# Kernel optimization log

Hardware: AMD Instinct MI355X
Metric: run time of the kernel (lower is better)

The kernel has to match this reference:

```python
import jax, jax.numpy as jnp
import numpy as np

M, L, D, V = 4096, 15, 1024, 32  # moves, word_max, in_sz, vocab_sz


def setup_inputs() -> dict:
    key = jax.random.key(0)
    ks = jax.random.split(key, 9)
    s = 0.02
    return {
        "tokens": jax.random.randint(ks[0], (M, L), 0, V),
        "letter_emb": jax.random.normal(ks[1], (V, D), jnp.float32) * s,
        "pos_emb": jax.random.normal(ks[2], (L, D), jnp.float32) * s,
        "Wq": jax.random.normal(ks[3], (D, D), jnp.float32) * s,
        "bq": jax.random.normal(ks[4], (D,), jnp.float32) * s,
        "Wk": jax.random.normal(ks[5], (D, D), jnp.float32) * s,
        "bk": jax.random.normal(ks[6], (D,), jnp.float32) * s,
        "Wv": jax.random.normal(ks[7], (D, D), jnp.float32) * s,
        "bv": jax.random.normal(ks[8], (D,), jnp.float32) * s,
    }


def reference(tokens, letter_emb, pos_emb, Wq, bq, Wk, bk, Wv, bv):
    # WordEncoder, batched across all M moves.
    x = letter_emb[tokens] + pos_emb[None, :, :]          # [M, L, D]
    q = jnp.einsum("mld,ed->mle", x, Wq) + bq             # Linear: x @ W.T + b
    k = jnp.einsum("mld,ed->mle", x, Wk) + bk
    v = jnp.einsum("mld,ed->mle", x, Wv) + bv
    scores = jax.nn.softmax(jnp.einsum("mle,mke->mlk", q, k), axis=-1)  # [M, L, L]
    attn = jnp.einsum("mlk,mke->mle", scores, v)          # [M, L, D]
    word = attn.sum(axis=1)                               # [M, D]
    # enc = word + ordered, where ordered is an identical second evaluation
    # of word_enc on the same word -> enc = 2 * word.
    return 2.0 * word
```

## Files before the change

kernel.cpp:

```cpp
#include <hip/hip_runtime.h>
#include <hip/hip_bf16.h>

#define NMOVES 4096
#define LW     15
#define DIM    1024
#define VOC    32
#define XROW   48
#define KSPL   4
#define GSPL   8
#define PLSZ   (48 * DIM)

typedef __attribute__((ext_vector_type(8))) short  short8;
typedef __attribute__((ext_vector_type(4))) float  floatx4;

__device__ __forceinline__ unsigned short f2b(float f) {
  unsigned int x;
  __builtin_memcpy(&x, &f, 4);
  x = x + 0x7FFFu + ((x >> 16) & 1u);
  return (unsigned short)(x >> 16);
}
__device__ __forceinline__ float b2f(unsigned short u) {
  unsigned int x = ((unsigned int)u) << 16;
  float f;
  __builtin_memcpy(&f, &x, 4);
  return f;
}
__device__ __forceinline__ short8 pk8(float4 a, float4 b) {
  short8 r;
  r[0] = (short)f2b(a.x); r[1] = (short)f2b(a.y);
  r[2] = (short)f2b(a.z); r[3] = (short)f2b(a.w);
  r[4] = (short)f2b(b.x); r[5] = (short)f2b(b.y);
  r[6] = (short)f2b(b.z); r[7] = (short)f2b(b.w);
  return r;
}
__device__ __forceinline__ float4 ld4(const float* p) {
  return *reinterpret_cast<const float4*>(p);
}

__global__ __launch_bounds__(256) void proj_ksplit(
    const float* __restrict__ letter, const float* __restrict__ pos,
    const float* __restrict__ Wq, const float* __restrict__ Wk,
    const float* __restrict__ Wv, float* __restrict__ Xp,
    float* __restrict__ G48) {
  const int tid = threadIdx.x;
  if (blockIdx.x == 0 && blockIdx.y == 0 && blockIdx.z == 0) {
#pragma unroll
    for (int i = 0; i < (XROW * 64) / 256; ++i) G48[i * 256 + tid] = 0.f;
  }

  const int p     = blockIdx.x;
  const int bn0   = blockIdx.y * 64;
  const int z     = blockIdx.z;
  const int kbase = p * 256;
  const float* W = (z == 0) ? Wq : (z == 1) ? Wk : Wv;
  float*       O = Xp + (size_t)(z * KSPL + p) * PLSZ;

  const int lane = tid & 63;
  const int wave = tid >> 6;
  const int wr   = wave >> 1;
  const int wc   = wave & 1;
  const int quad = lane >> 4;
  const int l16  = lane & 15;

  const int rA0 = wr * 32 + l16;
  const int rA1 = rA0 + 16;
  const float* a0p = (rA0 < 32) ? letter + (size_t)rA0 * DIM
                   : (rA0 < 47) ? pos + (size_t)(rA0 - 32) * DIM : nullptr;
  const float* a1p = (rA1 < 32) ? letter + (size_t)rA1 * DIM
                   : (rA1 < 47) ? pos + (size_t)(rA1 - 32) * DIM : nullptr;
  const float* b0p = W + (size_t)(bn0 + wc * 32 + l16) * DIM;
  const float* b1p = b0p + (size_t)16 * DIM;

  floatx4 acc[2][2];
#pragma unroll
  for (int i = 0; i < 2; ++i)
#pragma unroll
    for (int j = 0; j < 2; ++j) acc[i][j] = (floatx4){0.f, 0.f, 0.f, 0.f};

  const short8 z8 = (short8){0,0,0,0,0,0,0,0};
#pragma unroll
  for (int kk = 0; kk < 256; kk += 32) {
    const int kc = kbase + kk + quad * 8;
    short8 a0 = a0p ? pk8(ld4(a0p + kc), ld4(a0p + kc + 4)) : z8;
    short8 a1 = a1p ? pk8(ld4(a1p + kc), ld4(a1p + kc + 4)) : z8;
    short8 b0 = pk8(ld4(b0p + kc), ld4(b0p + kc + 4));
    short8 b1 = pk8(ld4(b1p + kc), ld4(b1p + kc + 4));
    acc[0][0] = __builtin_amdgcn_mfma_f32_16x16x32_bf16(a0, b0, acc[0][0], 0, 0, 0);
    acc[0][1] = __builtin_amdgcn_mfma_f32_16x16x32_bf16(a0, b1, acc[0][1], 0, 0, 0);
    acc[1][0] = __builtin_amdgcn_mfma_f32_16x16x32_bf16(a1, b0, acc[1][0], 0, 0, 0);
    acc[1][1] = __builtin_amdgcn_mfma_f32_16x16x32_bf16(a1, b1, acc[1][1], 0, 0, 0);
  }

#pragma unroll
  for (int mi = 0; mi < 2; ++mi) {
#pragma unroll
    for (int ni = 0; ni < 2; ++ni) {
      const int gcol = bn0 + wc * 32 + ni * 16 + l16;
#pragma unroll
      for (int i = 0; i < 4; ++i) {
        const int grow = wr * 32 + mi * 16 + quad * 4 + i;
        if (grow < 47)
          O[(size_t)grow * DIM + gcol] = acc[mi][ni][i];
      }
    }
  }
}

__device__ __forceinline__ short8 gfrag(const float* __restrict__ X4,
                                        const float* __restrict__ bias,
                                        int row, int kc) {
  if (row < 47) {
    const float* r0 = X4 + (size_t)row * DIM + kc;
    float4 s0 = ld4(r0),            s1 = ld4(r0 + 4);
    float4 t0 = ld4(r0 + PLSZ),     t1 = ld4(r0 + PLSZ + 4);
    float4 u0 = ld4(r0 + 2 * PLSZ), u1 = ld4(r0 + 2 * PLSZ + 4);
    float4 v0 = ld4(r0 + 3 * PLSZ), v1 = ld4(r0 + 3 * PLSZ + 4);
    s0.x += t0.x + u0.x + v0.x; s0.y += t0.y + u0.y + v0.y;
    s0.z += t0.z + u0.z + v0.z; s0.w += t0.w + u0.w + v0.w;
    s1.x += t1.x + u1.x + v1.x; s1.y += t1.y + u1.y + v1.y;
    s1.z += t1.z + u1.z + v1.z; s1.w += t1.w + u1.w + v1.w;
    return pk8(s0, s1);
  } else if (row == 47) {
    return pk8(ld4(bias + kc), ld4(bias + kc + 4));
  }
  return (short8){0,0,0,0,0,0,0,0};
}

__global__ __launch_bounds__(256) void gram_vexp(
    const float* __restrict__ Xp,
    const float* __restrict__ bq, const float* __restrict__ bk,
    float* __restrict__ G48, unsigned short* __restrict__ XvT) {
  const int bid = blockIdx.x;
  const int tid = threadIdx.x;

  if (bid < GSPL) {
    const int kbase = bid * 128;
    const int lane = tid & 63;
    const int wave = tid >> 6;
    const int wr   = wave >> 1;
    const int wc   = wave & 1;
    const int quad = lane >> 4;
    const int l16  = lane & 15;

    const float* Xq4 = Xp;
    const float* Xk4 = Xp + (size_t)4 * PLSZ;
    const int rA0 = wr * 32 + l16, rA1 = rA0 + 16;
    const int rB0 = wc * 32 + l16, rB1 = rB0 + 16;

    floatx4 acc[2][2];
#pragma unroll
    for (int i = 0; i < 2; ++i)
#pragma unroll
      for (int j = 0; j < 2; ++j) acc[i][j] = (floatx4){0.f, 0.f, 0.f, 0.f};

#pragma unroll
    for (int kk = 0; kk < 128; kk += 32) {
      const int kc = kbase + kk + quad * 8;
      short8 a0 = gfrag(Xq4, bq, rA0, kc);
      short8 a1 = gfrag(Xq4, bq, rA1, kc);
      short8 b0 = gfrag(Xk4, bk, rB0, kc);
      short8 b1 = gfrag(Xk4, bk, rB1, kc);
      acc[0][0] = __builtin_amdgcn_mfma_f32_16x16x32_bf16(a0, b0, acc[0][0], 0, 0, 0);
      acc[0][1] = __builtin_amdgcn_mfma_f32_16x16x32_bf16(a0, b1, acc[0][1], 0, 0, 0);
      acc[1][0] = __builtin_amdgcn_mfma_f32_16x16x32_bf16(a1, b0, acc[1][0], 0, 0, 0);
      acc[1][1] = __builtin_amdgcn_mfma_f32_16x16x32_bf16(a1, b1, acc[1][1], 0, 0, 0);
    }

#pragma unroll
    for (int mi = 0; mi < 2; ++mi) {
#pragma unroll
      for (int ni = 0; ni < 2; ++ni) {
        const int gcol = wc * 32 + ni * 16 + l16;
#pragma unroll
        for (int i = 0; i < 4; ++i) {
          const int grow = wr * 32 + mi * 16 + quad * 4 + i;
          if (grow < XROW)
            atomicAdd(&G48[(size_t)grow * 64 + gcol], acc[mi][ni][i]);
        }
      }
    }
  } else {
    const int n  = (bid - GSPL) * 64 + (tid & 63);
    const int kg = tid >> 6;
    const float* Xv4 = Xp + (size_t)8 * PLSZ;
#pragma unroll
    for (int s = 0; s < 4; ++s) {
      const int k0 = kg * 4 + s * 16;
      ushort4 o;
      unsigned short* oc = &o.x;
#pragma unroll
      for (int i = 0; i < 4; ++i) {
        const int k = k0 + i;
        float v = 0.f;
        if (k < 47) {
          const size_t off = (size_t)k * DIM + n;
          v = Xv4[off] + Xv4[off + PLSZ] + Xv4[off + 2 * PLSZ] +
              Xv4[off + 3 * PLSZ];
        }
        oc[i] = f2b(v);
      }
      *reinterpret_cast<ushort4*>(XvT + (size_t)n * 64 + k0) = o;
    }
  }
}

__global__ __launch_bounds__(256) void attn_gemm(
    const void* __restrict__ tokens_raw, const float* __restrict__ G48,
    const unsigned short* __restrict__ XvT, const float* __restrict__ bv,
    float* __restrict__ out) {
  __shared__ float Gs[XROW * 65];
  __shared__ float Sm[16][LW][17];
  __shared__ float CL[16][64];
  __shared__ __attribute__((aligned(16))) unsigned short CLh[16 * 72];
  __shared__ __attribute__((aligned(16))) unsigned short CLl[16 * 72];
  __shared__ int   tokL[16][16];
  __shared__ int   is64_s;
  const int m0  = blockIdx.x * 16;
  const int cb0 = blockIdx.y * 256;
  const int tid = threadIdx.x;

  const unsigned int* u32 = (const unsigned int*)tokens_raw;
  if (tid < 64) {
    unsigned int v = u32[2 * tid + 1];
    unsigned long long nz = __ballot(v != 0);
    if (tid == 0) is64_s = (nz == 0ULL) ? 1 : 0;
  }
#pragma unroll
  for (int i = 0; i < 12; ++i) {
    const int idx = i * 256 + tid;
    Gs[(idx >> 6) * 65 + (idx & 63)] = G48[idx];
  }
  {
    const int g = tid >> 4, L = tid & 15;
#pragma unroll
    for (int i = 0; i < 4; ++i) CL[g][L * 4 + i] = 0.f;
  }
  __syncthreads();

  if (tid < 16 * LW) {
    const int mv = tid / LW, j = tid - mv * LW;
    int t;
    if (is64_s) t = (int)((const long long*)tokens_raw)[(size_t)(m0 + mv) * LW + j];
    else        t = ((const int*)tokens_raw)[(size_t)(m0 + mv) * LW + j];
    tokL[mv][j] = t;
  }
  __syncthreads();

  const int g = tid >> 4;
  const int L = tid & 15;
  if (L < LW) {
    const int rb0 = tokL[g][L] * 65;
    const int rb1 = (32 + L) * 65;
    const int rb2 = (XROW - 1) * 65;
    float S[LW];
#pragma unroll
    for (int j = 0; j < LW; ++j) {
      const int c0 = tokL[g][j];
      const int c1 = 32 + j;
      S[j] = Gs[rb0 + c0] + Gs[rb1 + c0] + Gs[rb2 + c0]
           + Gs[rb0 + c1] + Gs[rb1 + c1] + Gs[rb2 + c1];
    }
    float mx = S[0];
#pragma unroll
    for (int j = 1; j < LW; ++j) mx = fmaxf(mx, S[j]);
    float sum = 0.f;
#pragma unroll
    for (int j = 0; j < LW; ++j) { S[j] = __expf(S[j] - mx); sum += S[j]; }
    const float inv = 1.0f / sum;
#pragma unroll
    for (int j = 0; j < LW; ++j) Sm[g][L][j] = S[j] * inv;
  }
  __syncthreads();

  if (L < LW) {
    float s = 0.f;
#pragma unroll
    for (int l = 0; l < LW; ++l) s += Sm[g][l][L];
    const float wj = 2.0f * s;
    atomicAdd(&CL[g][tokL[g][L]], wj);
    CL[g][32 + L] = wj;
  }
  __syncthreads();

  {
    float4 cv = *reinterpret_cast<const float4*>(&CL[g][L * 4]);
    ushort4 hi, lo;
    hi.x = f2b(cv.x); hi.y = f2b(cv.y); hi.z = f2b(cv.z); hi.w = f2b(cv.w);
    lo.x = f2b(cv.x - b2f(hi.x)); lo.y = f2b(cv.y - b2f(hi.y));
    lo.z = f2b(cv.z - b2f(hi.z)); lo.w = f2b(cv.w - b2f(hi.w));
    *reinterpret_cast<ushort4*>(CLh + g * 72 + L * 4) = hi;
    *reinterpret_cast<ushort4*>(CLl + g * 72 + L * 4) = lo;
  }
  __syncthreads();

  const int lane = tid & 63;
  const int wave = tid >> 6;
  const int quad = lane >> 4;
  const int l16  = lane & 15;
  const int colb = cb0 + wave * 64;

  floatx4 acc[4];
#pragma unroll
  for (int i = 0; i < 4; ++i) acc[i] = (floatx4){0.f, 0.f, 0.f, 0.f};

#pragma unroll
  for (int ks = 0; ks < 64; ks += 32) {
    short8 ah = *reinterpret_cast<const short8*>(CLh + l16 * 72 + ks + quad * 8);
    short8 al = *reinterpret_cast<const short8*>(CLl + l16 * 72 + ks + quad * 8);
#pragma unroll
    for (int ni = 0; ni < 4; ++ni) {
      const unsigned short* B = XvT + (size_t)(colb + ni * 16 + l16) * 64;
      short8 b = *reinterpret_cast<const short8*>(B + ks + quad * 8);
      acc[ni] = __builtin_amdgcn_mfma_f32_16x16x32_bf16(ah, b, acc[ni], 0, 0, 0);
      acc[ni] = __builtin_amdgcn_mfma_f32_16x16x32_bf16(al, b, acc[ni], 0, 0, 0);
    }
  }

#pragma unroll
  for (int ni = 0; ni < 4; ++ni) {
    const int gcol = colb + ni * 16 + l16;
    const float bias30 = 30.0f * bv[gcol];
#pragma unroll
    for (int i = 0; i < 4; ++i) {
      out[(size_t)(m0 + quad * 4 + i) * DIM + gcol] = acc[ni][i] + bias30;
    }
  }
}

extern "C" void kernel_launch(void* const* d_in, const int* in_sizes, int n_in,
                              void* d_out, int out_size, void* d_ws, size_t ws_size,
                              hipStream_t stream) {
  const void*  tokens = d_in[0];
  const float* letter = (const float*)d_in[1];
  const float* pos    = (const float*)d_in[2];
  const float* Wq     = (const float*)d_in[3];
  const float* bq     = (const float*)d_in[4];
  const float* Wk     = (const float*)d_in[5];
  const float* bk     = (const float*)d_in[6];
  const float* Wv     = (const float*)d_in[7];
  const float* bv     = (const float*)d_in[8];
  float*       outp   = (float*)d_out;

  char* ws = (char*)d_ws;
  const size_t XP_SZ  = (size_t)12 * PLSZ * 4;
  const size_t G_SZ   = (size_t)XROW * 64 * 4;
  float*          Xp  = (float*)(ws);
  float*          Gp  = (float*)(ws + XP_SZ);
  unsigned short* XvT = (unsigned short*)(ws + XP_SZ + G_SZ);

  proj_ksplit<<<dim3(KSPL, 16, 3), 256, 0, stream>>>(letter, pos, Wq, Wk, Wv,
                                                     Xp, Gp);
  gram_vexp<<<GSPL + 16, 256, 0, stream>>>(Xp, bq, bk, Gp, XvT);
  attn_gemm<<<dim3(NMOVES / 16, 4), 256, 0, stream>>>(tokens, Gp, XvT, bv, outp);
}
```

Before: 113.9 us.

## Fuse projection and gram kernels with a grid-wide atomic barrier

Merges the k-split projection kernel and the gram/V-transpose kernel into one launch. Producer blocks increment a global counter after writing partial projections, and consumer blocks spin until all 192 producers are done. This removes one kernel launch and the inter-kernel gap. The cost is spin-wait overhead, and it relies on all blocks being co-resident. The counter reset combined with persistent magic words may race across repeated calls.

Measured after the change: 121.5 us. 1.07x slower.

```diff
diff --git a/kernel.cpp b/kernel.cpp
--- a/kernel.cpp
+++ b/kernel.cpp
@@ -9,6 +9,7 @@
 #define KSPL   4
 #define GSPL   8
 #define PLSZ   (48 * DIM)
+#define ARM_MAGIC 0xA17C0DE1u
 
 typedef __attribute__((ext_vector_type(8))) short  short8;
 typedef __attribute__((ext_vector_type(4))) float  floatx4;
@@ -35,75 +36,6 @@
 }
 __device__ __forceinline__ float4 ld4(const float* p) {
   return *reinterpret_cast<const float4*>(p);
-}
-
-__global__ __launch_bounds__(256) void proj_ksplit(
-    const float* __restrict__ letter, const float* __restrict__ pos,
-    const float* __restrict__ Wq, const float* __restrict__ Wk,
-    const float* __restrict__ Wv, float* __restrict__ Xp,
-    float* __restrict__ G48) {
-  const int tid = threadIdx.x;
-  if (blockIdx.x == 0 && blockIdx.y == 0 && blockIdx.z == 0) {
-#pragma unroll
-    for (int i = 0; i < (XROW * 64) / 256; ++i) G48[i * 256 + tid] = 0.f;
-  }
-
-  const int p     = blockIdx.x;
-  const int bn0   = blockIdx.y * 64;
-  const int z     = blockIdx.z;
-  const int kbase = p * 256;
-  const float* W = (z == 0) ? Wq : (z == 1) ? Wk : Wv;
-  float*       O = Xp + (size_t)(z * KSPL + p) * PLSZ;
-
-  const int lane = tid & 63;
-  const int wave = tid >> 6;
-  const int wr   = wave >> 1;
-  const int wc   = wave & 1;
-  const int quad = lane >> 4;
-  const int l16  = lane & 15;
-
-  const int rA0 = wr * 32 + l16;
-  const int rA1 = rA0 + 16;
-  const float* a0p = (rA0 < 32) ? letter + (size_t)rA0 * DIM
-                   : (rA0 < 47) ? pos + (size_t)(rA0 - 32) * DIM : nullptr;
-  const float* a1p = (rA1 < 32) ? letter + (size_t)rA1 * DIM
-                   : (rA1 < 47) ? pos + (size_t)(rA1 - 32) * DIM : nullptr;
-  const float* b0p = W + (size_t)(bn0 + wc * 32 + l16) * DIM;
-  const float* b1p = b0p + (size_t)16 * DIM;
-
-  floatx4 acc[2][2];
-#pragma unroll
-  for (int i = 0; i < 2; ++i)
-#pragma unroll
-    for (int j = 0; j < 2; ++j) acc[i][j] = (floatx4){0.f, 0.f, 0.f, 0.f};
-
-  const short8 z8 = (short8){0,0,0,0,0,0,0,0};
-#pragma unroll
-  for (int kk = 0; kk < 256; kk += 32) {
-    const int kc = kbase + kk + quad * 8;
-    short8 a0 = a0p ? pk8(ld4(a0p + kc), ld4(a0p + kc + 4)) : z8;
-    short8 a1 = a1p ? pk8(ld4(a1p + kc), ld4(a1p + kc + 4)) : z8;
-    short8 b0 = pk8(ld4(b0p + kc), ld4(b0p + kc + 4));
-    short8 b1 = pk8(ld4(b1p + kc), ld4(b1p + kc + 4));
-    acc[0][0] = __builtin_amdgcn_mfma_f32_16x16x32_bf16(a0, b0, acc[0][0], 0, 0, 0);
-    acc[0][1] = __builtin_amdgcn_mfma_f32_16x16x32_bf16(a0, b1, acc[0][1], 0, 0, 0);
-    acc[1][0] = __builtin_amdgcn_mfma_f32_16x16x32_bf16(a1, b0, acc[1][0], 0, 0, 0);
-    acc[1][1] = __builtin_amdgcn_mfma_f32_16x16x32_bf16(a1, b1, acc[1][1], 0, 0, 0);
-  }
-
-#pragma unroll
-  for (int mi = 0; mi < 2; ++mi) {
-#pragma unroll
-    for (int ni = 0; ni < 2; ++ni) {
-      const int gcol = bn0 + wc * 32 + ni * 16 + l16;
-#pragma unroll
-      for (int i = 0; i < 4; ++i) {
-        const int grow = wr * 32 + mi * 16 + quad * 4 + i;
-        if (grow < 47)
-          O[(size_t)grow * DIM + gcol] = acc[mi][ni][i];
-      }
-    }
-  }
 }
 
 __device__ __forceinline__ short8 gfrag(const float* __restrict__ X4,
@@ -126,15 +58,37 @@
   return (short8){0,0,0,0,0,0,0,0};
 }
 
-__global__ __launch_bounds__(256) void gram_vexp(
-    const float* __restrict__ Xp,
+__global__ __launch_bounds__(256) void proj_gram(
+    const float* __restrict__ letter, const float* __restrict__ pos,
+    const float* __restrict__ Wq, const float* __restrict__ Wk,
+    const float* __restrict__ Wv,
     const float* __restrict__ bq, const float* __restrict__ bk,
-    float* __restrict__ G48, unsigned short* __restrict__ XvT) {
+    float* __restrict__ Xp, float* __restrict__ G48,
+    unsigned short* __restrict__ XvT, unsigned int* __restrict__ syncw) {
   const int bid = blockIdx.x;
   const int tid = threadIdx.x;
 
-  if (bid < GSPL) {
-    const int kbase = bid * 128;
+  if (bid < 192) {
+    if (bid == 0) {
+#pragma unroll
+      for (int i = 0; i < (XROW * 64) / 256; ++i) G48[i * 256 + tid] = 0.f;
+      __syncthreads();
+      if (tid == 0) {
+        atomicExch(&syncw[0], 0u);
+        __threadfence();
+        atomicExch(&syncw[2], ARM_MAGIC);
+        atomicExch(&syncw[3], ~ARM_MAGIC);
+      }
+    }
+
+    const int p  = bid & 3;
+    const int ny = (bid >> 2) & 15;
+    const int z  = bid >> 6;
+    const int kbase = p * 256;
+    const int bn0   = ny * 64;
+    const float* W = (z == 0) ? Wq : (z == 1) ? Wk : Wv;
+    float*       O = Xp + (size_t)(z * KSPL + p) * PLSZ;
+
     const int lane = tid & 63;
     const int wave = tid >> 6;
     const int wr   = wave >> 1;
@@ -142,10 +96,14 @@
     const int quad = lane >> 4;
     const int l16  = lane & 15;
 
-    const float* Xq4 = Xp;
-    const float* Xk4 = Xp + (size_t)4 * PLSZ;
-    const int rA0 = wr * 32 + l16, rA1 = rA0 + 16;
-    const int rB0 = wc * 32 + l16, rB1 = rB0 + 16;
+    const int rA0 = wr * 32 + l16;
+    const int rA1 = rA0 + 16;
+    const float* a0p = (rA0 < 32) ? letter + (size_t)rA0 * DIM
+                     : (rA0 < 47) ? pos + (size_t)(rA0 - 32) * DIM : nullptr;
+    const float* a1p = (rA1 < 32) ? letter + (size_t)rA1 * DIM
+                     : (rA1 < 47) ? pos + (size_t)(rA1 - 32) * DIM : nullptr;
+    const float* b0p = W + (size_t)(bn0 + wc * 32 + l16) * DIM;
+    const float* b1p = b0p + (size_t)16 * DIM;
 
     floatx4 acc[2][2];
 #pragma unroll
@@ -153,13 +111,14 @@
 #pragma unroll
       for (int j = 0; j < 2; ++j) acc[i][j] = (floatx4){0.f, 0.f, 0.f, 0.f};
 
-#pragma unroll
-    for (int kk = 0; kk < 128; kk += 32) {
+    const short8 z8 = (short8){0,0,0,0,0,0,0,0};
+#pragma unroll
+    for (int kk = 0; kk < 256; kk += 32) {
       const int kc = kbase + kk + quad * 8;
-      short8 a0 = gfrag(Xq4, bq, rA0, kc);
-      short8 a1 = gfrag(Xq4, bq, rA1, kc);
-      short8 b0 = gfrag(Xk4, bk, rB0, kc);
-      short8 b1 = gfrag(Xk4, bk, rB1, kc);
+      short8 a0 = a0p ? pk8(ld4(a0p + kc), ld4(a0p + kc + 4)) : z8;
+      short8 a1 = a1p ? pk8(ld4(a1p + kc), ld4(a1p + kc + 4)) : z8;
+      short8 b0 = pk8(ld4(b0p + kc), ld4(b0p + kc + 4));
+      short8 b1 = pk8(ld4(b1p + kc), ld4(b1p + kc + 4));
       acc[0][0] = __builtin_amdgcn_mfma_f32_16x16x32_bf16(a0, b0, acc[0][0], 0, 0, 0);
       acc[0][1] = __builtin_amdgcn_mfma_f32_16x16x32_bf16(a0, b1, acc[0][1], 0, 0, 0);
       acc[1][0] = __builtin_amdgcn_mfma_f32_16x16x32_bf16(a1, b0, acc[1][0], 0, 0, 0);
@@ -170,36 +129,101 @@
     for (int mi = 0; mi < 2; ++mi) {
 #pragma unroll
       for (int ni = 0; ni < 2; ++ni) {
-        const int gcol = wc * 32 + ni * 16 + l16;
+        const int gcol = bn0 + wc * 32 + ni * 16 + l16;
 #pragma unroll
         for (int i = 0; i < 4; ++i) {
           const int grow = wr * 32 + mi * 16 + quad * 4 + i;
-          if (grow < XROW)
-            atomicAdd(&G48[(size_t)grow * 64 + gcol], acc[mi][ni][i]);
+          if (grow < 47)
+            O[(size_t)grow * DIM + gcol] = acc[mi][ni][i];
         }
       }
     }
+
+    __syncthreads();
+    if (tid == 0) {
+      while (atomicAdd(&syncw[2], 0u) != ARM_MAGIC ||
+             atomicAdd(&syncw[3], 0u) != ~ARM_MAGIC) { }
+      __threadfence();
+      atomicAdd(&syncw[0], 1u);
+    }
   } else {
-    const int n  = (bid - GSPL) * 64 + (tid & 63);
-    const int kg = tid >> 6;
-    const float* Xv4 = Xp + (size_t)8 * PLSZ;
-#pragma unroll
-    for (int s = 0; s < 4; ++s) {
-      const int k0 = kg * 4 + s * 16;
-      ushort4 o;
-      unsigned short* oc = &o.x;
-#pragma unroll
-      for (int i = 0; i < 4; ++i) {
-        const int k = k0 + i;
-        float v = 0.f;
-        if (k < 47) {
-          const size_t off = (size_t)k * DIM + n;
-          v = Xv4[off] + Xv4[off + PLSZ] + Xv4[off + 2 * PLSZ] +
-              Xv4[off + 3 * PLSZ];
+    if (tid == 0) {
+      while (atomicAdd(&syncw[2], 0u) != ARM_MAGIC ||
+             atomicAdd(&syncw[3], 0u) != ~ARM_MAGIC) { }
+      while (atomicAdd(&syncw[0], 0u) < 192u) { }
+      __threadfence();
+    }
+    __syncthreads();
+
+    const int cb = bid - 192;
+    if (cb < GSPL) {
+      const int kbase = cb * 128;
+      const int lane = tid & 63;
+      const int wave = tid >> 6;
+      const int wr   = wave >> 1;
+      const int wc   = wave & 1;
+      const int quad = lane >> 4;
+      const int l16  = lane & 15;
+
+      const float* Xq4 = Xp;
+      const float* Xk4 = Xp + (size_t)4 * PLSZ;
+      const int rA0 = wr * 32 + l16, rA1 = rA0 + 16;
+      const int rB0 = wc * 32 + l16, rB1 = rB0 + 16;
+
+      floatx4 acc[2][2];
+#pragma unroll
+      for (int i = 0; i < 2; ++i)
+#pragma unroll
+        for (int j = 0; j < 2; ++j) acc[i][j] = (floatx4){0.f, 0.f, 0.f, 0.f};
+
+#pragma unroll
+      for (int kk = 0; kk < 128; kk += 32) {
+        const int kc = kbase + kk + quad * 8;
+        short8 a0 = gfrag(Xq4, bq, rA0, kc);
+        short8 a1 = gfrag(Xq4, bq, rA1, kc);
+        short8 b0 = gfrag(Xk4, bk, rB0, kc);
+        short8 b1 = gfrag(Xk4, bk, rB1, kc);
+        acc[0][0] = __builtin_amdgcn_mfma_f32_16x16x32_bf16(a0, b0, acc[0][0], 0, 0, 0);
+        acc[0][1] = __builtin_amdgcn_mfma_f32_16x16x32_bf16(a0, b1, acc[0][1], 0, 0, 0);
+        acc[1][0] = __builtin_amdgcn_mfma_f32_16x16x32_bf16(a1, b0, acc[1][0], 0, 0, 0);
+        acc[1][1] = __builtin_amdgcn_mfma_f32_16x16x32_bf16(a1, b1, acc[1][1], 0, 0, 0);
+      }
+
+#pragma unroll
+      for (int mi = 0; mi < 2; ++mi) {
+#pragma unroll
+        for (int ni = 0; ni < 2; ++ni) {
+          const int gcol = wc * 32 + ni * 16 + l16;
+#pragma unroll
+          for (int i = 0; i < 4; ++i) {
+            const int grow = wr * 32 + mi * 16 + quad * 4 + i;
+            if (grow < XROW)
+              atomicAdd(&G48[(size_t)grow * 64 + gcol], acc[mi][ni][i]);
+          }
         }
-        oc[i] = f2b(v);
-      }
-      *reinterpret_cast<ushort4*>(XvT + (size_t)n * 64 + k0) = o;
+      }
+    } else {
+      const int n  = (cb - GSPL) * 64 + (tid & 63);
+      const int kg = tid >> 6;
+      const float* Xv4 = Xp + (size_t)8 * PLSZ;
+#pragma unroll
+      for (int s = 0; s < 4; ++s) {
+        const int k0 = kg * 4 + s * 16;
+        ushort4 o;
+        unsigned short* oc = &o.x;
+#pragma unroll
+        for (int i = 0; i < 4; ++i) {
+          const int k = k0 + i;
+          float v = 0.f;
+          if (k < 47) {
+            const size_t off = (size_t)k * DIM + n;
+            v = Xv4[off] + Xv4[off + PLSZ] + Xv4[off + 2 * PLSZ] +
+                Xv4[off + 3 * PLSZ];
+          }
+          oc[i] = f2b(v);
+        }
+        *reinterpret_cast<ushort4*>(XvT + (size_t)n * 64 + k0) = o;
+      }
     }
   }
 }
@@ -344,12 +368,13 @@
   char* ws = (char*)d_ws;
   const size_t XP_SZ  = (size_t)12 * PLSZ * 4;
   const size_t G_SZ   = (size_t)XROW * 64 * 4;
-  float*          Xp  = (float*)(ws);
-  float*          Gp  = (float*)(ws + XP_SZ);
-  unsigned short* XvT = (unsigned short*)(ws + XP_SZ + G_SZ);
-
-  proj_ksplit<<<dim3(KSPL, 16, 3), 256, 0, stream>>>(letter, pos, Wq, Wk, Wv,
-                                                     Xp, Gp);
-  gram_vexp<<<GSPL + 16, 256, 0, stream>>>(Xp, bq, bk, Gp, XvT);
+  const size_t XVT_SZ = (size_t)DIM * 64 * 2;
+  float*          Xp    = (float*)(ws);
+  float*          Gp    = (float*)(ws + XP_SZ);
+  unsigned short* XvT   = (unsigned short*)(ws + XP_SZ + G_SZ);
+  unsigned int*   syncw = (unsigned int*)(ws + XP_SZ + G_SZ + XVT_SZ);
+
+  proj_gram<<<192 + GSPL + 16, 256, 0, stream>>>(letter, pos, Wq, Wk, Wv,
+                                                 bq, bk, Xp, Gp, XvT, syncw);
   attn_gemm<<<dim3(NMOVES / 16, 4), 256, 0, stream>>>(tokens, Gp, XvT, bv, outp);
 }
```
